# Kernel optimization log

Hardware: AMD Instinct MI355X
Metric: run time of the kernel (lower is better)

Reference implementation:

```python
import jax, jax.numpy as jnp
import numpy as np

D_MODEL = 1024
N_HEADS = 16
HEAD_DIM = D_MODEL // N_HEADS
ROPE_BASE = 10000.0


def _rope_cos_sin(seq_len, head_dim, dtype):
    inv_freq = 1.0 / (ROPE_BASE ** (jnp.arange(0, head_dim, 2, dtype=jnp.float32) / head_dim))
    t = jnp.arange(seq_len, dtype=jnp.float32)
    freqs = jnp.outer(t, inv_freq)            # [S, head_dim//2]
    emb = jnp.concatenate([freqs, freqs], axis=-1)  # [S, head_dim]
    return jnp.cos(emb).astype(dtype), jnp.sin(emb).astype(dtype)


def _rotate_half(x):
    half = x.shape[-1] // 2
    return jnp.concatenate([-x[..., half:], x[..., :half]], axis=-1)


def setup_inputs() -> dict:
    key = jax.random.key(0)
    k0, k1, k2, k3, k4 = jax.random.split(key, 5)
    B, S = 2, 2048
    scale = 1.0 / np.sqrt(D_MODEL)
    return {
        "hidden_states": jax.random.normal(k0, (B, S, D_MODEL), dtype=jnp.float32),
        "w_q": jax.random.normal(k1, (D_MODEL, D_MODEL), dtype=jnp.float32) * scale,
        "w_k": jax.random.normal(k2, (D_MODEL, D_MODEL), dtype=jnp.float32) * scale,
        "w_v": jax.random.normal(k3, (D_MODEL, D_MODEL), dtype=jnp.float32) * scale,
        "w_o": jax.random.normal(k4, (D_MODEL, D_MODEL), dtype=jnp.float32) * scale,
    }


def reference(hidden_states, w_q, w_k, w_v, w_o):
    B, S, D = hidden_states.shape
    H, hd = N_HEADS, HEAD_DIM

    def proj(w):
        # nn.Linear: x @ w.T -> [B, H, S, hd]
        return (hidden_states @ w.T).reshape(B, S, H, hd).transpose(0, 2, 1, 3)

    q, k, v = proj(w_q), proj(w_k), proj(w_v)

    cos, sin = _rope_cos_sin(S, hd, hidden_states.dtype)
    cos = cos[None, None]  # [1,1,S,hd]
    sin = sin[None, None]
    q = q * cos + _rotate_half(q) * sin
    k = k * cos + _rotate_half(k) * sin

    scores = jnp.einsum("bhqd,bhkd->bhqk", q, k) / jnp.sqrt(jnp.asarray(hd, hidden_states.dtype))
    attn = jax.nn.softmax(scores, axis=-1)
    out = jnp.einsum("bhqk,bhkd->bhqd", attn, v)
    out = out.transpose(0, 2, 1, 3).reshape(B, S, D)
    return out @ w_o.T
```

## Files before the change

### kernel.cpp

```cpp
#include <hip/hip_runtime.h>
#include <math.h>

#define SEQ 2048
#define NTOK 4096
#define DM 1024

typedef __bf16 bf16x8 __attribute__((ext_vector_type(8)));
typedef __bf16 bf16x4 __attribute__((ext_vector_type(4)));
typedef float  f32x4  __attribute__((ext_vector_type(4)));

__device__ __forceinline__ void gll16(const void* g, void* l) {
    __builtin_amdgcn_global_load_lds(
        (const __attribute__((address_space(1))) void*)g,
        (__attribute__((address_space(3))) void*)l, 16, 0, 0);
}

__device__ __forceinline__ f32x4 mfma16(bf16x8 a, bf16x8 b, f32x4 c) {
    return __builtin_amdgcn_mfma_f32_16x16x32_bf16(a, b, c, 0, 0, 0);
}

__global__ void rope_tables(float* __restrict__ ct, float* __restrict__ st) {
    int idx = blockIdx.x * 256 + threadIdx.x;
    int s = idx >> 6, d = idx & 63;
    int e = d & 31;
    float invf = 1.0f / powf(10000.0f, (float)e / 32.0f);
    float ang  = (float)s * invf;
    double a   = (double)ang;
    ct[s * 64 + d] = (float)cos(a);
    st[s * 64 + d] = (float)sin(a);
}

__global__ void conv_all(const float* __restrict__ hs, const float* __restrict__ wq,
                         const float* __restrict__ wk, const float* __restrict__ wv,
                         const float* __restrict__ wo, __bf16* hsb, __bf16* wqb,
                         __bf16* wkb, __bf16* wvb, __bf16* wob) {
    long i = (long)blockIdx.x * 256 + threadIdx.x;
    const long H4 = (long)NTOK * DM / 4;
    const float* src; __bf16* dst; long off;
    if (i < H4) { src = hs; dst = hsb; off = i; }
    else {
        long t = i - H4;
        int wsel = (int)(t >> 18);
        off = t & ((1L << 18) - 1);
        switch (wsel) {
            case 0:  src = wq; dst = wqb; break;
            case 1:  src = wk; dst = wkb; break;
            case 2:  src = wv; dst = wvb; break;
            default: src = wo; dst = wob; break;
        }
    }
    float4 v = ((const float4*)src)[off];
    __bf16* o = dst + off * 4;
    o[0] = (__bf16)v.x; o[1] = (__bf16)v.y; o[2] = (__bf16)v.z; o[3] = (__bf16)v.w;
}

template <typename OutT, bool ROPE>
__device__ __forceinline__ void gemm_core(__bf16* __restrict__ L,
                                          const __bf16* __restrict__ A,
                                          const __bf16* __restrict__ B,
                                          OutT* __restrict__ C, int N, float scale,
                                          const float* __restrict__ ct,
                                          const float* __restrict__ st,
                                          long bm, long bn) {
    const int tid  = threadIdx.x;
    const int lane = tid & 63;
    const int wid  = tid >> 6;
    const int l15  = lane & 15, lg = lane >> 4;
    const int wr = (wid >> 1) * 64, wc = (wid & 1) * 64;

    f32x4 acc[4][4];
    #pragma unroll
    for (int i = 0; i < 4; ++i)
        #pragma unroll
        for (int j = 0; j < 4; ++j) acc[i][j] = 0;

    const int i0 = tid, i1 = tid + 256;
    const __bf16* Ag0 = A + (bm + (i0 >> 2)) * 1024 + (((i0 & 3) ^ ((i0 >> 3) & 3)) * 8);
    const __bf16* Ag1 = A + (bm + (i1 >> 2)) * 1024 + (((i1 & 3) ^ ((i1 >> 3) & 3)) * 8);
    const __bf16* Bg0 = B + (bn + (i0 >> 2)) * 1024 + (((i0 & 3) ^ ((i0 >> 3) & 3)) * 8);
    const __bf16* Bg1 = B + (bn + (i1 >> 2)) * 1024 + (((i1 & 3) ^ ((i1 >> 3) & 3)) * 8);

    auto stage = [&](int buf, int k0) {
        gll16(Ag0 + k0, &L[buf * 8192 + tid * 8]);
        gll16(Ag1 + k0, &L[buf * 8192 + 2048 + tid * 8]);
        gll16(Bg0 + k0, &L[buf * 8192 + 4096 + tid * 8]);
        gll16(Bg1 + k0, &L[buf * 8192 + 6144 + tid * 8]);
    };

    const int rbase = l15 * 32 + ((lg ^ ((l15 >> 1) & 3)) * 8);

    auto compute = [&](int buf) {
        const int AS = buf * 8192, BS = buf * 8192 + 4096;
        bf16x8 a[4], b[4];
        #pragma unroll
        for (int i = 0; i < 4; ++i)
            a[i] = *(const bf16x8*)(L + AS + (wr + i * 16) * 32 + rbase);
        #pragma unroll
        for (int j = 0; j < 4; ++j)
            b[j] = *(const bf16x8*)(L + BS + (wc + j * 16) * 32 + rbase);
        __builtin_amdgcn_s_setprio(1);
        #pragma unroll
        for (int i = 0; i < 4; ++i)
            #pragma unroll
            for (int j = 0; j < 4; ++j)
                acc[i][j] = mfma16(a[i], b[j], acc[i][j]);
        __builtin_amdgcn_s_setprio(0);
    };

    stage(0, 0);
    __syncthreads();
    #pragma unroll 1
    for (int t = 0; t < 32; t += 2) {
        stage(1, (t + 1) * 32);
        compute(0);
        __syncthreads();
        if (t + 2 < 32) stage(0, (t + 2) * 32);
        compute(1);
        __syncthreads();
    }

    if constexpr (ROPE) {
        #pragma unroll
        for (int i = 0; i < 4; ++i)
            #pragma unroll
            for (int j = 0; j < 2; ++j)
                #pragma unroll
                for (int r = 0; r < 4; ++r) {
                    long row = bm + wr + i * 16 + lg * 4 + r;
                    int  s   = (int)(row & (SEQ - 1));
                    int  d   = j * 16 + l15;
                    float c  = ct[s * 64 + d];
                    float sn = st[s * 64 + d];
                    float x0 = acc[i][j][r], x1 = acc[i][j + 2][r];
                    long col = bn + wc + j * 16 + l15;
                    C[row * N + col]      = (OutT)((x0 * c - x1 * sn) * scale);
                    C[row * N + col + 32] = (OutT)((x1 * c + x0 * sn) * scale);
                }
    } else {
        #pragma unroll
        for (int i = 0; i < 4; ++i)
            #pragma unroll
            for (int j = 0; j < 4; ++j)
                #pragma unroll
                for (int r = 0; r < 4; ++r) {
                    long row = bm + wr + i * 16 + lg * 4 + r;
                    long col = bn + wc + j * 16 + l15;
                    C[row * N + col] = (OutT)(acc[i][j][r] * scale);
                }
    }
}

__global__ __launch_bounds__(256) void gemm_qkv(const __bf16* __restrict__ hsb,
                                                const __bf16* __restrict__ wqb,
                                                const __bf16* __restrict__ wkb,
                                                const __bf16* __restrict__ wvb,
                                                __bf16* __restrict__ Qb,
                                                __bf16* __restrict__ Kb,
                                                __bf16* __restrict__ Vtb,
                                                const float* __restrict__ ct,
                                                const float* __restrict__ st) {
    __shared__ __bf16 L[16384];
    const int bid = blockIdx.x;
    const int w = (bid & 7) * 96 + (bid >> 3);
    const int z = w >> 8, rem = w & 255;
    if (z == 0)
        gemm_core<__bf16, true>(L, hsb, wqb, Qb, 1024, 0.125f, ct, st,
                                (long)(rem >> 3) * 128, (long)(rem & 7) * 128);
    else if (z == 1)
        gemm_core<__bf16, true>(L, hsb, wkb, Kb, 1024, 1.0f, ct, st,
                                (long)(rem >> 3) * 128, (long)(rem & 7) * 128);
    else
        gemm_core<__bf16, false>(L, wvb, hsb, Vtb, 4096, 1.0f, nullptr, nullptr,
                                 (long)(rem & 7) * 128, (long)(rem >> 3) * 128);
}

__global__ __launch_bounds__(256) void gemm_out(const __bf16* __restrict__ A,
                                                const __bf16* __restrict__ B,
                                                float* __restrict__ C) {
    __shared__ __bf16 L[16384];
    const int bid = blockIdx.x;
    const int w = (bid & 7) * 32 + (bid >> 3);
    gemm_core<float, false>(L, A, B, C, 1024, 1.0f, nullptr, nullptr,
                            (long)(w >> 3) * 128, (long)(w & 7) * 128);
}

#define FIXED_M 16.0f

__global__ __launch_bounds__(512) void flash9(const __bf16* __restrict__ Qb,
                                              const __bf16* __restrict__ Kb,
                                              const __bf16* __restrict__ Vt,
                                              __bf16* __restrict__ Ob) {
    __shared__ __bf16 L[24576];
    const int h = blockIdx.x, b = blockIdx.y, qt = blockIdx.z;
    const int tid = threadIdx.x, lane = tid & 63, w = tid >> 6;
    const int wq = w >> 1, wk = w & 1;
    const int l15 = lane & 15, lg = lane >> 4;

    const int x7  = l15 & 7;
    const int kb0 = wk * 2048 + l15 * 64 + ((lg ^ x7) * 8);
    const int kb1 = wk * 2048 + l15 * 64 + (((4 + lg) ^ x7) * 8);
    const int vb0 = l15 * 64 + (((wk * 4 + lg) ^ x7) * 8);
    const int prb = 16384 + (wq * 32 + l15) * 64 + (((wk * 4 + lg) ^ x7) * 8);
    int wb[2];
    #pragma unroll
    for (int j = 0; j < 2; ++j)
        wb[j] = 16384 + (wq * 32 + l15) * 64 +
                (((wk * 4 + j * 2 + (lg >> 1)) ^ x7) * 8) + (lg & 1) * 4;

    bf16x8 qf[2][2];
    #pragma unroll
    for (int qa = 0; qa < 2; ++qa) {
        long qrow = (long)b * SEQ + qt * 128 + wq * 32 + qa * 16 + l15;
        qf[qa][0] = *(const bf16x8*)(Qb + qrow * DM + h * 64 + lg * 8);
        qf[qa][1] = *(const bf16x8*)(Qb + qrow * DM + h * 64 + 32 + lg * 8);
    }

    f32x4 oacc[2][4];
    #pragma unroll
    for (int qa = 0; qa < 2; ++qa)
        #pragma unroll
        for (int i = 0; i < 4; ++i) oacc[qa][i] = 0;
    f32x4 lvec[2] = {0, 0};

    const int srow = tid >> 3;
    const int sgz  = (tid & 7) ^ (srow & 7);
    const __bf16* kp = Kb + ((long)b * SEQ + srow) * DM + h * 64 + sgz * 8;
    const __bf16* vp = Vt + ((long)h * 64 + srow) * NTOK + (long)b * SEQ + sgz * 8;

    auto stage = [&](int bf) {
        gll16(kp, &L[bf * 4096 + tid * 8]);
        gll16(vp, &L[8192 + bf * 4096 + tid * 8]);
        kp += (long)64 * DM;
        vp += 64;
    };

    const float L2E = 1.4426950408889634f;
    const float mL  = FIXED_M * L2E;

    auto compute = [&](int bf) {
        const int KS = bf * 4096, VS = 8192 + bf * 4096;
        f32x4 sc[2][2];
        __builtin_amdgcn_s_setprio(1);
        #pragma unroll
        for (int j = 0; j < 2; ++j) {
            bf16x8 ka0 = *(const bf16x8*)(L + KS + j * 1024 + kb0);
            bf16x8 ka1 = *(const bf16x8*)(L + KS + j * 1024 + kb1);
            #pragma unroll
            for (int qa = 0; qa < 2; ++qa) {
                f32x4 z = 0;
                z = mfma16(ka0, qf[qa][0], z);
                z = mfma16(ka1, qf[qa][1], z);
                sc[qa][j] = z;
            }
        }
        __builtin_amdgcn_s_setprio(0);

        #pragma unroll
        for (int qa = 0; qa < 2; ++qa) {
            f32x4 rv = 0;
            #pragma unroll
            for (int j = 0; j < 2; ++j) {
                #pragma unroll
                for (int r = 0; r < 4; ++r)
                    sc[qa][j][r] = __builtin_amdgcn_exp2f(
                        __builtin_fmaf(sc[qa][j][r], L2E, -mL));
                rv += sc[qa][j];
            }
            lvec[qa] += rv;
            #pragma unroll
            for (int j = 0; j < 2; ++j) {
                bf16x4 p4;
                p4[0] = (__bf16)sc[qa][j][0]; p4[1] = (__bf16)sc[qa][j][1];
                p4[2] = (__bf16)sc[qa][j][2]; p4[3] = (__bf16)sc[qa][j][3];
                *(bf16x4*)(L + wb[j] + qa * 1024) = p4;
            }
        }

        bf16x8 pb[2];
        #pragma unroll
        for (int qa = 0; qa < 2; ++qa)
            pb[qa] = *(const bf16x8*)(L + prb + qa * 1024);
        __builtin_amdgcn_s_setprio(1);
        #pragma unroll
        for (int i = 0; i < 4; ++i) {
            bf16x8 vb = *(const bf16x8*)(L + VS + i * 1024 + vb0);
            #pragma unroll
            for (int qa = 0; qa < 2; ++qa)
                oacc[qa][i] = mfma16(vb, pb[qa], oacc[qa][i]);
        }
        __builtin_amdgcn_s_setprio(0);
    };

    stage(0);
    __syncthreads();

    #pragma unroll 1
    for (int t = 0; t < 32; t += 2) {
        stage(1);
        compute(0);
        __syncthreads();
        if (t + 2 < 32) stage(0);
        compute(1);
        __syncthreads();
    }

    float lh[2];
    #pragma unroll
    for (int qa = 0; qa < 2; ++qa) {
        float l = (lvec[qa][0] + lvec[qa][1]) + (lvec[qa][2] + lvec[qa][3]);
        l += __shfl_xor(l, 16);
        l += __shfl_xor(l, 32);
        lh[qa] = l;
    }

    float* df = (float*)L;
    float* lf = df + 9216;
    if (wk) {
        const int base = (wq * 64 + lane) * 36;
        #pragma unroll
        for (int qa = 0; qa < 2; ++qa) {
            #pragma unroll
            for (int i = 0; i < 4; ++i)
                *(f32x4*)(df + base + qa * 16 + i * 4) = oacc[qa][i];
            if (lg == 0) lf[wq * 32 + qa * 16 + l15] = lh[qa];
        }
    }
    __syncthreads();
    if (!wk) {
        const int base = (wq * 64 + lane) * 36;
        #pragma unroll
        for (int qa = 0; qa < 2; ++qa) {
            float lt = lh[qa] + lf[wq * 32 + qa * 16 + l15];
            float linv = 1.0f / lt;
            const long tok = (long)b * SEQ + qt * 128 + wq * 32 + qa * 16 + l15;
            #pragma unroll
            for (int i = 0; i < 4; ++i) {
                f32x4 ot = oacc[qa][i] + *(const f32x4*)(df + base + qa * 16 + i * 4);
                bf16x4 o4;
                #pragma unroll
                for (int r = 0; r < 4; ++r) o4[r] = (__bf16)(ot[r] * linv);
                *(bf16x4*)(Ob + tok * DM + h * 64 + i * 16 + lg * 4) = o4;
            }
        }
    }
}

extern "C" void kernel_launch(void* const* d_in, const int* in_sizes, int n_in,
                              void* d_out, int out_size, void* d_ws, size_t ws_size,
                              hipStream_t stream) {
    const float* hs = (const float*)d_in[0];
    const float* wq = (const float*)d_in[1];
    const float* wk = (const float*)d_in[2];
    const float* wv = (const float*)d_in[3];
    const float* wo = (const float*)d_in[4];
    float* out = (float*)d_out;

    __bf16* hsb = (__bf16*)d_ws;
    __bf16* wqb = hsb + (long)NTOK * DM;
    __bf16* wkb = wqb + DM * DM;
    __bf16* wvb = wkb + DM * DM;
    __bf16* wob = wvb + DM * DM;
    __bf16* Qb  = wob + DM * DM;
    __bf16* Kb  = Qb + (long)NTOK * DM;
    __bf16* Vtb = Kb + (long)NTOK * DM;
    float*  ct  = (float*)(Vtb + (long)NTOK * DM);
    float*  st  = ct + SEQ * 64;

    rope_tables<<<dim3(SEQ * 64 / 256), 256, 0, stream>>>(ct, st);
    conv_all<<<dim3(8192), 256, 0, stream>>>(hs, wq, wk, wv, wo,
                                             hsb, wqb, wkb, wvb, wob);

    gemm_qkv<<<dim3(768), 256, 0, stream>>>(hsb, wqb, wkb, wvb,
                                            Qb, Kb, Vtb, ct, st);

    flash9<<<dim3(16, 2, SEQ / 128), 512, 0, stream>>>(Qb, Kb, Vtb, Qb);

    gemm_out<<<dim3(256), 256, 0, stream>>>(Qb, wob, out);
}
```

Measured before the change: 119.9 us.

## Triple-buffer GEMM K-loop with vmcnt waits, fold rope tables into conversion kernel

The GEMM main loop moves from double-buffered LDS with full __syncthreads to a three-stage ring. It prefetches two tiles ahead and uses s_waitcnt vmcnt plus raw barriers, so more global-to-LDS loads stay in flight during MFMA work. The rope table kernel is merged into the conversion launch as extra blocks, which saves one kernel launch. The Q scale of 0.125 is folded into the bf16 weight conversion, removing a per-output multiply. This costs more LDS per block (48KB), which may lower occupancy, and the exact vmcnt counting is fragile.

```diff
diff --git a/kernel.cpp b/kernel.cpp
--- a/kernel.cpp
+++ b/kernel.cpp
@@ -19,31 +19,33 @@
     return __builtin_amdgcn_mfma_f32_16x16x32_bf16(a, b, c, 0, 0, 0);
 }
 
-__global__ void rope_tables(float* __restrict__ ct, float* __restrict__ st) {
-    int idx = blockIdx.x * 256 + threadIdx.x;
-    int s = idx >> 6, d = idx & 63;
-    int e = d & 31;
-    float invf = 1.0f / powf(10000.0f, (float)e / 32.0f);
-    float ang  = (float)s * invf;
-    double a   = (double)ang;
-    ct[s * 64 + d] = (float)cos(a);
-    st[s * 64 + d] = (float)sin(a);
-}
-
 __global__ void conv_all(const float* __restrict__ hs, const float* __restrict__ wq,
                          const float* __restrict__ wk, const float* __restrict__ wv,
                          const float* __restrict__ wo, __bf16* hsb, __bf16* wqb,
-                         __bf16* wkb, __bf16* wvb, __bf16* wob) {
+                         __bf16* wkb, __bf16* wvb, __bf16* wob,
+                         float* __restrict__ ct, float* __restrict__ st) {
+    if (blockIdx.x >= 8192) {
+        int t = (blockIdx.x - 8192) * 256 + threadIdx.x;
+        int s = t >> 6, d = t & 63;
+        int e = d & 31;
+        float invf = 1.0f / powf(10000.0f, (float)e / 32.0f);
+        float ang  = (float)s * invf;
+        double a   = (double)ang;
+        ct[s * 64 + d] = (float)cos(a);
+        st[s * 64 + d] = (float)sin(a);
+        return;
+    }
     long i = (long)blockIdx.x * 256 + threadIdx.x;
     const long H4 = (long)NTOK * DM / 4;
     const float* src; __bf16* dst; long off;
+    float scale = 1.0f;
     if (i < H4) { src = hs; dst = hsb; off = i; }
     else {
         long t = i - H4;
         int wsel = (int)(t >> 18);
         off = t & ((1L << 18) - 1);
         switch (wsel) {
-            case 0:  src = wq; dst = wqb; break;
+            case 0:  src = wq; dst = wqb; scale = 0.125f; break;
             case 1:  src = wk; dst = wkb; break;
             case 2:  src = wv; dst = wvb; break;
             default: src = wo; dst = wob; break;
@@ -51,14 +53,15 @@
     }
     float4 v = ((const float4*)src)[off];
     __bf16* o = dst + off * 4;
-    o[0] = (__bf16)v.x; o[1] = (__bf16)v.y; o[2] = (__bf16)v.z; o[3] = (__bf16)v.w;
+    o[0] = (__bf16)(v.x * scale); o[1] = (__bf16)(v.y * scale);
+    o[2] = (__bf16)(v.z * scale); o[3] = (__bf16)(v.w * scale);
 }
 
 template <typename OutT, bool ROPE>
 __device__ __forceinline__ void gemm_core(__bf16* __restrict__ L,
                                           const __bf16* __restrict__ A,
                                           const __bf16* __restrict__ B,
-                                          OutT* __restrict__ C, int N, float scale,
+                                          OutT* __restrict__ C, int N,
                                           const float* __restrict__ ct,
                                           const float* __restrict__ st,
                                           long bm, long bn) {
@@ -108,16 +111,33 @@
     };
 
     stage(0, 0);
-    __syncthreads();
+    stage(1, 32);
+
     #pragma unroll 1
-    for (int t = 0; t < 32; t += 2) {
-        stage(1, (t + 1) * 32);
-        compute(0);
-        __syncthreads();
-        if (t + 2 < 32) stage(0, (t + 2) * 32);
-        compute(1);
-        __syncthreads();
-    }
+    for (int tt = 0; tt < 30; tt += 3) {
+        asm volatile("s_waitcnt vmcnt(4)" ::: "memory");
+        __builtin_amdgcn_s_barrier();
+        __builtin_amdgcn_sched_barrier(0);
+        stage(2, (tt + 2) * 32); compute(0);
+
+        asm volatile("s_waitcnt vmcnt(4)" ::: "memory");
+        __builtin_amdgcn_s_barrier();
+        __builtin_amdgcn_sched_barrier(0);
+        stage(0, (tt + 3) * 32); compute(1);
+
+        asm volatile("s_waitcnt vmcnt(4)" ::: "memory");
+        __builtin_amdgcn_s_barrier();
+        __builtin_amdgcn_sched_barrier(0);
+        stage(1, (tt + 4) * 32); compute(2);
+    }
+    asm volatile("s_waitcnt vmcnt(4)" ::: "memory");
+    __builtin_amdgcn_s_barrier();
+    __builtin_amdgcn_sched_barrier(0);
+    compute(0);
+    asm volatile("s_waitcnt vmcnt(0)" ::: "memory");
+    __builtin_amdgcn_s_barrier();
+    __builtin_amdgcn_sched_barrier(0);
+    compute(1);
 
     if constexpr (ROPE) {
         #pragma unroll
@@ -133,8 +153,8 @@
                     float sn = st[s * 64 + d];
                     float x0 = acc[i][j][r], x1 = acc[i][j + 2][r];
                     long col = bn + wc + j * 16 + l15;
-                    C[row * N + col]      = (OutT)((x0 * c - x1 * sn) * scale);
-                    C[row * N + col + 32] = (OutT)((x1 * c + x0 * sn) * scale);
+                    C[row * N + col]      = (OutT)(x0 * c - x1 * sn);
+                    C[row * N + col + 32] = (OutT)(x1 * c + x0 * sn);
                 }
     } else {
         #pragma unroll
@@ -145,7 +165,7 @@
                 for (int r = 0; r < 4; ++r) {
                     long row = bm + wr + i * 16 + lg * 4 + r;
                     long col = bn + wc + j * 16 + l15;
-                    C[row * N + col] = (OutT)(acc[i][j][r] * scale);
+                    C[row * N + col] = (OutT)acc[i][j][r];
                 }
     }
 }
@@ -159,28 +179,25 @@
                                                 __bf16* __restrict__ Vtb,
                                                 const float* __restrict__ ct,
                                                 const float* __restrict__ st) {
-    __shared__ __bf16 L[16384];
+    __shared__ __bf16 L[24576];
     const int bid = blockIdx.x;
     const int w = (bid & 7) * 96 + (bid >> 3);
     const int z = w >> 8, rem = w & 255;
-    if (z == 0)
-        gemm_core<__bf16, true>(L, hsb, wqb, Qb, 1024, 0.125f, ct, st,
-                                (long)(rem >> 3) * 128, (long)(rem & 7) * 128);
-    else if (z == 1)
-        gemm_core<__bf16, true>(L, hsb, wkb, Kb, 1024, 1.0f, ct, st,
+    if (z < 2)
+        gemm_core<__bf16, true>(L, hsb, z ? wkb : wqb, z ? Kb : Qb, 1024, ct, st,
                                 (long)(rem >> 3) * 128, (long)(rem & 7) * 128);
     else
-        gemm_core<__bf16, false>(L, wvb, hsb, Vtb, 4096, 1.0f, nullptr, nullptr,
+        gemm_core<__bf16, false>(L, wvb, hsb, Vtb, 4096, nullptr, nullptr,
                                  (long)(rem & 7) * 128, (long)(rem >> 3) * 128);
 }
 
 __global__ __launch_bounds__(256) void gemm_out(const __bf16* __restrict__ A,
                                                 const __bf16* __restrict__ B,
                                                 float* __restrict__ C) {
-    __shared__ __bf16 L[16384];
+    __shared__ __bf16 L[24576];
     const int bid = blockIdx.x;
     const int w = (bid & 7) * 32 + (bid >> 3);
-    gemm_core<float, false>(L, A, B, C, 1024, 1.0f, nullptr, nullptr,
+    gemm_core<float, false>(L, A, B, C, 1024, nullptr, nullptr,
                             (long)(w >> 3) * 128, (long)(w & 7) * 128);
 }
 
@@ -366,9 +383,8 @@
     float*  ct  = (float*)(Vtb + (long)NTOK * DM);
     float*  st  = ct + SEQ * 64;
 
-    rope_tables<<<dim3(SEQ * 64 / 256), 256, 0, stream>>>(ct, st);
-    conv_all<<<dim3(8192), 256, 0, stream>>>(hs, wq, wk, wv, wo,
-                                             hsb, wqb, wkb, wvb, wob);
+    conv_all<<<dim3(8704), 256, 0, stream>>>(hs, wq, wk, wv, wo,
+                                             hsb, wqb, wkb, wvb, wob, ct, st);
 
     gemm_qkv<<<dim3(768), 256, 0, stream>>>(hsb, wqb, wkb, wvb,
                                             Qb, Kb, Vtb, ct, st);
```

Result: faster. 106.3 us, median of 2 (-11.4%).
